# Performance work log

Measured on AMD Instinct MI355X. Metric: run time of the kernel, lower is better.

Reference implementation:

```python
import jax, jax.numpy as jnp
import numpy as np
from jax import lax

GN_EPS = 1e-5
LRELU_SLOPE = 0.2
TOP_K = 3
COMMITMENT = 0.25
NUM_CODES = 1024

def conv(x, w, b, stride=1, pad=1):
    y = lax.conv_general_dilated(x, w, (stride, stride), ((pad, pad), (pad, pad)),
                                 dimension_numbers=('NCHW', 'OIHW', 'NCHW'))
    return y + b[None, :, None, None]

def conv_transpose(x, w, b, stride=2, pad=1, out_pad=1):
    # torch ConvTranspose2d: w is (Cin, Cout, kH, kW); equivalent to lhs-dilated conv
    # with flipped, io-swapped kernel and padding k-1-p (plus out_pad on high side).
    k = w.shape[2]
    p = k - 1 - pad
    w_f = jnp.transpose(jnp.flip(w, (2, 3)), (1, 0, 2, 3))  # -> OIHW
    y = lax.conv_general_dilated(x, w_f, (1, 1), ((p, p + out_pad), (p, p + out_pad)),
                                 lhs_dilation=(stride, stride),
                                 dimension_numbers=('NCHW', 'OIHW', 'NCHW'))
    return y + b[None, :, None, None]

def group_norm(x, g, beta, groups=2):
    N, C, H, W = x.shape
    xg = x.reshape(N, groups, C // groups, H, W)
    mu = xg.mean((2, 3, 4), keepdims=True)
    var = xg.var((2, 3, 4), keepdims=True)
    xn = ((xg - mu) * lax.rsqrt(var + GN_EPS)).reshape(N, C, H, W)
    return xn * g[None, :, None, None] + beta[None, :, None, None]

def lrelu(x):
    return jnp.where(x >= 0, x, LRELU_SLOPE * x)

def vq_ema_eval(z, emb):
    # z: [B, D, H, W] -> tokens [N, D]; eval path (no EMA buffer updates)
    inputs = jnp.transpose(z, (0, 2, 3, 1))  # [B,H,W,D]
    flat = inputs.reshape(-1, emb.shape[1])
    d = (jnp.sum(flat ** 2, 1, keepdims=True) + jnp.sum(emb ** 2, 1)
         - 2.0 * flat @ emb.T)  # [N, K]
    _, idx = lax.top_k(-d, TOP_K)  # top_k smallest distances
    q0 = emb[idx[:, 0]].reshape(inputs.shape)
    e_latent_loss = jnp.mean((lax.stop_gradient(q0) - inputs) ** 2)
    loss = COMMITMENT * e_latent_loss
    quantized = inputs + lax.stop_gradient(q0 - inputs)  # straight-through
    # perplexity uses the LAST (k-th nearest) encodings, matching the torch loop
    last = idx[:, TOP_K - 1]
    counts = jnp.zeros((emb.shape[0],), flat.dtype).at[last].add(1.0)
    avg_probs = counts / flat.shape[0]
    perplexity = jnp.exp(-jnp.sum(avg_probs * jnp.log(avg_probs + 1e-10)))
    return loss, jnp.transpose(quantized, (0, 3, 1, 2)), perplexity

def setup_inputs() -> dict:
    key = jax.random.key(0)
    ks = jax.random.split(key, 16)
    s = 0.05
    d = {
        'x': jax.random.normal(ks[0], (4, 4, 96, 96), jnp.float32),
        'e0_w': jax.random.normal(ks[1], (128, 4, 3, 3), jnp.float32) * s,
        'e0_b': jnp.zeros((128,), jnp.float32),
        'e0_g': jnp.ones((128,), jnp.float32),
        'e0_beta': jnp.zeros((128,), jnp.float32),
        'e1_w': jax.random.normal(ks[2], (128, 128, 3, 3), jnp.float32) * s,
        'e1_b': jnp.zeros((128,), jnp.float32),
        'e1_g': jnp.ones((128,), jnp.float32),
        'e1_beta': jnp.zeros((128,), jnp.float32),
        'pv_w': jax.random.normal(ks[3], (128, 128, 1, 1), jnp.float32) * s,
        'pv_b': jnp.zeros((128,), jnp.float32),
        'emb': jax.random.normal(ks[4], (NUM_CODES, 128), jnp.float32),
        'd0_w': jax.random.normal(ks[5], (128, 128, 3, 3), jnp.float32) * s,  # ConvT: (Cin,Cout,k,k)
        'd0_b': jnp.zeros((128,), jnp.float32),
        'd0_g': jnp.ones((128,), jnp.float32),
        'd0_beta': jnp.zeros((128,), jnp.float32),
        'd1_w': jax.random.normal(ks[6], (128, 256, 3, 3), jnp.float32) * s,
        'd1_b': jnp.zeros((128,), jnp.float32),
        'd1_g': jnp.ones((128,), jnp.float32),
        'd1_beta': jnp.zeros((128,), jnp.float32),
        'proj_w': jax.random.normal(ks[7], (128, 128, 1, 1), jnp.float32) * s,
        'proj_b': jnp.zeros((128,), jnp.float32),
        'ro_w': jax.random.normal(ks[8], (4, 128, 1, 1), jnp.float32) * s,
        'ro_b': jnp.zeros((4,), jnp.float32),
    }
    return d

def reference(x, e0_w, e0_b, e0_g, e0_beta, e1_w, e1_b, e1_g, e1_beta,
              pv_w, pv_b, emb,
              d0_w, d0_b, d0_g, d0_beta, d1_w, d1_b, d1_g, d1_beta,
              proj_w, proj_b, ro_w, ro_b):
    # Encoder: strides [1, 2]
    enc1 = lrelu(group_norm(conv(x, e0_w, e0_b, stride=1, pad=1), e0_g, e0_beta))
    latent = lrelu(group_norm(conv(enc1, e1_w, e1_b, stride=2, pad=1), e1_g, e1_beta))
    z = conv(latent, pv_w, pv_b, stride=1, pad=0)
    loss, quantized, perplexity = vq_ema_eval(z, emb)
    # Decoder: strides [2, 1]; skip projected (embedding_dim != C_out)
    skip = conv(enc1, proj_w, proj_b, stride=1, pad=0)
    h = lrelu(group_norm(conv_transpose(quantized, d0_w, d0_b, stride=2, pad=1, out_pad=1), d0_g, d0_beta))
    y = lrelu(group_norm(conv(jnp.concatenate([h, skip], axis=1), d1_w, d1_b, stride=1, pad=1), d1_g, d1_beta))
    x_recon = conv(y, ro_w, ro_b, stride=1, pad=0)
    return (loss, x_recon, perplexity)
```

## Files before the change

### kernel.cpp

```cpp
#include <hip/hip_runtime.h>

#define DEVI __device__ __forceinline__

typedef unsigned short u16;
typedef __attribute__((ext_vector_type(8))) short bf8v;
typedef __attribute__((ext_vector_type(4))) short s4v;
typedef __attribute__((ext_vector_type(4))) float f4v;

constexpr int NB = 4, C = 128, H = 96, W = 96, HW = H * W;
constexpr int HL = 48, WL = 48, HWL = HL * WL;
constexpr int CODES = 1024, DIM = 128;
constexpr int ROWS = NB * HWL;

DEVI float lrelu_f(float v) { return v >= 0.f ? v : 0.2f * v; }

DEVI u16 f2bf(float f) {
  union { float f; unsigned u; } v; v.f = f;
  unsigned r = (v.u + 0x7FFFu + ((v.u >> 16) & 1u)) >> 16;
  return (u16)r;
}

DEVI float bf2f(u16 h) {
  union { unsigned u; float f; } v; v.u = (unsigned)h << 16;
  return v.f;
}

DEVI void wave_red2(float& s, float& s2) {
#pragma unroll
  for (int o = 32; o > 0; o >>= 1) { s += __shfl_down(s, o); s2 += __shfl_down(s2, o); }
}

DEVI bool block_red2(float& s, float& s2) {
  wave_red2(s, s2);
  __shared__ float ls[8], ls2[8];
  int wv = threadIdx.x >> 6, ln = threadIdx.x & 63;
  if (ln == 0) { ls[wv] = s; ls2[wv] = s2; }
  __syncthreads();
  if (threadIdx.x == 0) {
    s = ls[0] + ls[1] + ls[2] + ls[3];
    s2 = ls2[0] + ls2[1] + ls2[2] + ls2[3];
    return true;
  }
  return false;
}

DEVI void ins3(float e, int j, float& d0, int& i0, float& d1, int& i1, float& d2, int& i2) {
  bool b0 = (e < d0) || (e == d0 && j < i0);
  bool b1 = (e < d1) || (e == d1 && j < i1);
  bool b2 = (e < d2) || (e == d2 && j < i2);
  float nd0 = b0 ? e : d0;             int ni0 = b0 ? j : i0;
  float nd1 = b0 ? d0 : (b1 ? e : d1); int ni1 = b0 ? i0 : (b1 ? j : i1);
  float nd2 = b1 ? d1 : (b2 ? e : d2); int ni2 = b1 ? i1 : (b2 ? j : i2);
  d0 = nd0; i0 = ni0; d1 = nd1; i1 = ni1; d2 = nd2; i2 = ni2;
}

__global__ __launch_bounds__(256) void k_red16(const float2* __restrict__ src,
                                               float* __restrict__ dst, int per) {
  int slot = blockIdx.x;
  float s = 0.f, s2 = 0.f;
  for (int i = threadIdx.x; i < per; i += 256) {
    float2 v = src[(size_t)slot * per + i];
    s += v.x; s2 += v.y;
  }
  if (block_red2(s, s2)) { dst[slot * 2] = s; dst[slot * 2 + 1] = s2; }
}

__global__ __launch_bounds__(256) void k_pack_all(
    const float* __restrict__ d1_w, const float* __restrict__ d0_w,
    const float* __restrict__ pj_w, const float* __restrict__ emb,
    u16* __restrict__ A1, u16* __restrict__ A0, u16* __restrict__ Apj,
    u16* __restrict__ ehlp, float* __restrict__ enorm, float* __restrict__ counts) {
  int b = blockIdx.x, t = threadIdx.x;
  if (b < 1152) {
    int i = b * 256 + t;
    int ci = i & 31, co = (i >> 5) & 127, r = i >> 12;
    int kx = r % 3; int r2 = r / 3; int ch = r2 & 7, ky = r2 >> 3;
    A1[i] = f2bf(d1_w[((size_t)(co * 256 + ch * 32 + ci) * 3 + ky) * 3 + kx]);
  } else if (b < 1728) {
    int i = (b - 1152) * 256 + t;
    int ci = i & 31, co = (i >> 5) & 127, r = i >> 12;
    int wx = r % 3; int r2 = r / 3; int ch = r2 & 3, wy = r2 >> 2;
    A0[i] = f2bf(d0_w[((size_t)((ch * 32 + ci) * 128 + co) * 3 + wy) * 3 + wx]);
  } else if (b < 1792) {
    int i = (b - 1728) * 256 + t;
    int ci = i & 31, co = (i >> 5) & 127, ch = i >> 12;
    Apj[i] = f2bf(pj_w[co * 128 + ch * 32 + ci]);
  } else if (b < 1920) {
    int i = (b - 1792) * 256 + t;
    int k4 = i & 31, code = i >> 5;
    float4 e = *(const float4*)&emb[(size_t)code * DIM + k4 * 4];
    u16 h0 = f2bf(e.x), h1 = f2bf(e.y), h2 = f2bf(e.z), h3 = f2bf(e.w);
    u16 l0 = f2bf(e.x - bf2f(h0)), l1 = f2bf(e.y - bf2f(h1));
    u16 l2 = f2bf(e.z - bf2f(h2)), l3 = f2bf(e.w - bf2f(h3));
    s4v hv = {(short)h0, (short)h1, (short)h2, (short)h3};
    s4v lv = {(short)l0, (short)l1, (short)l2, (short)l3};
    *(s4v*)&ehlp[(size_t)code * 256 + k4 * 4] = hv;
    *(s4v*)&ehlp[(size_t)code * 256 + 128 + k4 * 4] = lv;
  } else if (b < 1924) {
    int e = (b - 1920) * 256 + t;
    const float4* p = (const float4*)(emb + (size_t)e * DIM);
    float s = 0.f;
#pragma unroll 8
    for (int i = 0; i < 32; ++i) {
      float4 v = p[i];
      s = fmaf(v.x, v.x, s); s = fmaf(v.y, v.y, s); s = fmaf(v.z, v.z, s); s = fmaf(v.w, v.w, s);
    }
    enorm[e] = s;
  } else {
#pragma unroll
    for (int k = 0; k < 4; ++k) counts[t + k * 256] = 0.f;
  }
}

__global__ __launch_bounds__(256) void k_conv_e0t(
    const float* __restrict__ x, const float* __restrict__ wg,
    const float* __restrict__ bias, float* __restrict__ out, float2* __restrict__ ps) {
  __shared__ float xs[4][18][104];
  int b = blockIdx.x;
  int rq = b % 6; int co = (b / 6) & 127; int n = b / 768;
  int t = threadIdx.x;
  int tx = t & 15, r = t >> 4;
  int y0 = rq * 16;
  for (int e = t; e < 4 * 18 * 104; e += 256) {
    int ci = e / 1872; int rem = e - ci * 1872;
    int row = rem / 104; int off = rem - row * 104;
    int iy = y0 - 1 + row; int ix = off - 1;
    float v = 0.f;
    if ((unsigned)iy < 96u && (unsigned)ix < 96u)
      v = x[((size_t)(n * 4 + ci)) * HW + iy * 96 + ix];
    xs[ci][row][off] = v;
  }
  float wr[4][9];
  const float* wp = wg + co * 36;
#pragma unroll
  for (int ci = 0; ci < 4; ++ci)
#pragma unroll
    for (int k = 0; k < 9; ++k) wr[ci][k] = wp[ci * 9 + k];
  float bv = bias[co];
  __syncthreads();
  float acc[6];
#pragma unroll
  for (int p = 0; p < 6; ++p) acc[p] = bv;
#pragma unroll
  for (int ci = 0; ci < 4; ++ci) {
#pragma unroll
    for (int ky = 0; ky < 3; ++ky) {
      const float* rp = &xs[ci][r + ky][6 * tx];
      float f[8];
#pragma unroll
      for (int j = 0; j < 4; ++j) {
        float2 v2 = *(const float2*)(rp + 2 * j);
        f[2 * j] = v2.x; f[2 * j + 1] = v2.y;
      }
      float w0 = wr[ci][ky * 3 + 0], w1 = wr[ci][ky * 3 + 1], w2 = wr[ci][ky * 3 + 2];
#pragma unroll
      for (int p = 0; p < 6; ++p)
        acc[p] = fmaf(w0, f[p], fmaf(w1, f[p + 1], fmaf(w2, f[p + 2], acc[p])));
    }
  }
  float* op = out + ((size_t)(n * 128 + co) * 96 + (y0 + r)) * 96 + 6 * tx;
#pragma unroll
  for (int j = 0; j < 3; ++j) {
    float2 v2 = { acc[2 * j], acc[2 * j + 1] };
    *(float2*)(op + 2 * j) = v2;
  }
  float s = 0.f, s2 = 0.f;
#pragma unroll
  for (int p = 0; p < 6; ++p) { s += acc[p]; s2 += acc[p] * acc[p]; }
  if (block_red2(s, s2)) {
    int slot = n * 2 + (co >> 6);
    ps[(size_t)slot * 384 + (co & 63) * 6 + rq] = make_float2(s, s2);
  }
}

__global__ __launch_bounds__(256) void k_gn_pad(
    const float* __restrict__ in, const float* __restrict__ stats,
    const float* __restrict__ gam, const float* __restrict__ bet, float* __restrict__ outp) {
  int idx = blockIdx.x * 256 + threadIdx.x;
  int col = idx % 100; int r2 = idx / 100; int row = r2 % 98; int c2 = r2 / 98;
  int c = c2 & 127; int n = c2 >> 7;
  float v = 0.f;
  if (row >= 1 && row <= 96 && col >= 1 && col <= 96) {
    const float* st = stats + (n * 2 + (c >> 6)) * 2;
    const float invc = 1.f / (64.f * 9216.f);
    float mu = st[0] * invc;
    float var = fmaf(-mu, mu, st[1] * invc);
    float rs = rsqrtf(var + 1e-5f);
    float raw = in[(size_t)c2 * 9216 + (row - 1) * 96 + (col - 1)];
    v = lrelu_f(fmaf((raw - mu) * rs, gam[c], bet[c]));
  }
  outp[idx] = v;
}

__global__ __launch_bounds__(256) void k_gn_nhwc_bf(
    const float* __restrict__ in, u16* __restrict__ outb, const float* __restrict__ stats,
    const float* __restrict__ gam, const float* __restrict__ bet) {
  int idx = blockIdx.x * 256 + threadIdx.x;
  int c = idx & 127;
  int n = idx / (9216 * 128);
  const float* st = stats + (n * 2 + (c >> 6)) * 2;
  const float invcnt = 1.f / (64.f * 9216.f);
  float mu = st[0] * invcnt;
  float var = fmaf(-mu, mu, st[1] * invcnt);
  float rs = rsqrtf(var + 1e-5f);
  float v = in[idx];
  outb[idx] = f2bf(lrelu_f(fmaf((v - mu) * rs, gam[c], bet[c])));
}

__global__ __launch_bounds__(256, 4) void k_conv_e1s(
    const float* __restrict__ gnpad, const float* __restrict__ wg, float* __restrict__ part) {
  __shared__ float insh[8 * 500];
  __shared__ float wsh[8 * 576];
  int b = blockIdx.x;
  int cb = b & 1; int kb = (b >> 1) & 3; int rq = (b >> 3) % 24; int n = b / 192;
  int co0 = cb * 64;
  int t = threadIdx.x;
  int tx = t & 15, r = (t >> 4) & 1, cg = t >> 5;
  float acc[8][3];
#pragma unroll
  for (int c = 0; c < 8; ++c)
#pragma unroll
    for (int p = 0; p < 3; ++p) acc[c][p] = 0.f;
  for (int cc = 0; cc < 4; ++cc) {
    __syncthreads();
    const float4* src = (const float4*)(gnpad + ((size_t)(n * 128 + kb * 32 + cc * 8)) * 9800 + 4 * rq * 100);
#pragma unroll
    for (int j = 0; j < 4; ++j) {
      int e = t + j * 256;
      if (e < 1000) {
        int ci = e / 125; int q = e - ci * 125;
        *(float4*)&insh[ci * 500 + q * 4] = src[(size_t)ci * 2450 + q];
      }
    }
#pragma unroll
    for (int j = 0; j < 18; ++j) {
      int e = t + j * 256;
      int ci = e / 576; int rem = e - ci * 576; int k = rem >> 6; int co = rem & 63;
      wsh[e] = wg[(size_t)(co0 + co) * 1152 + (kb * 32 + cc * 8 + ci) * 9 + k];
    }
    __syncthreads();
#pragma unroll
    for (int ci = 0; ci < 8; ++ci) {
      float iv[3][3][3];
      int ib = ci * 500 + (2 * r) * 100 + 2 * tx;
#pragma unroll
      for (int ky = 0; ky < 3; ++ky) {
#pragma unroll
        for (int p = 0; p < 3; ++p) {
          int a = ib + ky * 100 + 32 * p;
          float2 v2 = *(const float2*)&insh[a];
          iv[ky][p][0] = v2.x; iv[ky][p][1] = v2.y; iv[ky][p][2] = insh[a + 2];
        }
      }
#pragma unroll
      for (int k = 0; k < 9; ++k) {
        float4 wa = *(const float4*)&wsh[ci * 576 + k * 64 + cg * 8];
        float4 wb = *(const float4*)&wsh[ci * 576 + k * 64 + cg * 8 + 4];
        int ky = k / 3, kx = k - ky * 3;
#pragma unroll
        for (int p = 0; p < 3; ++p) {
          float ivv = iv[ky][p][kx];
          acc[0][p] = fmaf(wa.x, ivv, acc[0][p]);
          acc[1][p] = fmaf(wa.y, ivv, acc[1][p]);
          acc[2][p] = fmaf(wa.z, ivv, acc[2][p]);
          acc[3][p] = fmaf(wa.w, ivv, acc[3][p]);
          acc[4][p] = fmaf(wb.x, ivv, acc[4][p]);
          acc[5][p] = fmaf(wb.y, ivv, acc[5][p]);
          acc[6][p] = fmaf(wb.z, ivv, acc[6][p]);
          acc[7][p] = fmaf(wb.w, ivv, acc[7][p]);
        }
      }
    }
  }
  int oy = 2 * rq + r;
#pragma unroll
  for (int c = 0; c < 8; ++c) {
    size_t ob = (size_t)kb * 1179648 + ((size_t)(n * 128 + co0 + cg * 8 + c)) * HWL + oy * 48 + tx;
#pragma unroll
    for (int p = 0; p < 3; ++p) part[ob + 16 * p] = acc[c][p];
  }
}

__global__ __launch_bounds__(256) void k_e1comb(
    const float* __restrict__ part, const float* __restrict__ bias,
    float* __restrict__ latent, float2* __restrict__ ps) {
  int idx = blockIdx.x * 256 + threadIdx.x;
  int c = (idx / HWL) & 127;
  int n = idx / (HWL * 128);
  float v = part[idx] + part[idx + 1179648] + part[idx + 2 * 1179648] + part[idx + 3 * 1179648] + bias[c];
  latent[idx] = v;
  float s = v, s2 = v * v;
  if (block_red2(s, s2)) {
    int slot = n * 2 + (c >> 6);
    int j = blockIdx.x % 9;
    ps[(size_t)slot * 576 + (c & 63) * 9 + j] = make_float2(s, s2);
  }
}

__global__ __launch_bounds__(256, 2) void k_pv(
    const float* __restrict__ in, const float* __restrict__ w,
    const float* __restrict__ bias, const float* __restrict__ stats1,
    const float* __restrict__ gam, const float* __restrict__ bet,
    u16* __restrict__ zp) {
  int b = blockIdx.x;
  int pxb = b % 36; int cb = (b / 36) & 1; int n = b / 72;
  int t = threadIdx.x;
  int pxg = t & 7, cg = t >> 3;
  int px0 = pxb * 64 + pxg * 8;
  int cobase = cb * 64 + cg * 2;
  const float invc = 1.f / (64.f * 2304.f);
  float acc[2][8];
#pragma unroll
  for (int c = 0; c < 2; ++c) {
    float bv = bias[cobase + c];
#pragma unroll
    for (int p = 0; p < 8; ++p) acc[c][p] = bv;
  }
  const float* ipb = in + (size_t)n * 128 * HWL + px0;
  for (int ci0 = 0; ci0 < 128; ci0 += 4) {
    float inr[4][8];
#pragma unroll
    for (int i = 0; i < 4; ++i) {
      int c = ci0 + i;
      const float* st = stats1 + (n * 2 + (c >> 6)) * 2;
      float mu = st[0] * invc;
      float var = fmaf(-mu, mu, st[1] * invc);
      float rsv = rsqrtf(var + 1e-5f);
      float ga = gam[c], be = bet[c];
      const float* ip = ipb + (size_t)c * HWL;
      float4 a = *(const float4*)ip; float4 bq = *(const float4*)(ip + 4);
      inr[i][0] = lrelu_f(fmaf((a.x - mu) * rsv, ga, be));
      inr[i][1] = lrelu_f(fmaf((a.y - mu) * rsv, ga, be));
      inr[i][2] = lrelu_f(fmaf((a.z - mu) * rsv, ga, be));
      inr[i][3] = lrelu_f(fmaf((a.w - mu) * rsv, ga, be));
      inr[i][4] = lrelu_f(fmaf((bq.x - mu) * rsv, ga, be));
      inr[i][5] = lrelu_f(fmaf((bq.y - mu) * rsv, ga, be));
      inr[i][6] = lrelu_f(fmaf((bq.z - mu) * rsv, ga, be));
      inr[i][7] = lrelu_f(fmaf((bq.w - mu) * rsv, ga, be));
    }
    float wr[2][4];
#pragma unroll
    for (int c = 0; c < 2; ++c) {
      float4 wv = *(const float4*)&w[(size_t)(cobase + c) * 128 + ci0];
      wr[c][0] = wv.x; wr[c][1] = wv.y; wr[c][2] = wv.z; wr[c][3] = wv.w;
    }
#pragma unroll
    for (int i = 0; i < 4; ++i)
#pragma unroll
      for (int c = 0; c < 2; ++c)
#pragma unroll
        for (int p = 0; p < 8; ++p) acc[c][p] = fmaf(wr[c][i], inr[i][p], acc[c][p]);
  }
#pragma unroll
  for (int p = 0; p < 8; ++p) {
    size_t r = (size_t)n * HWL + px0 + p;
    u16 h0 = f2bf(acc[0][p]); u16 l0 = f2bf(acc[0][p] - bf2f(h0));
    u16 h1 = f2bf(acc[1][p]); u16 l1 = f2bf(acc[1][p] - bf2f(h1));
    unsigned hp = (unsigned)h0 | ((unsigned)h1 << 16);
    unsigned lp = (unsigned)l0 | ((unsigned)l1 << 16);
    *(unsigned*)&zp[r * 256 + cobase] = hp;
    *(unsigned*)&zp[r * 256 + 128 + cobase] = lp;
  }
}

__global__ __launch_bounds__(256) void k_vq(
    const u16* __restrict__ zp, const u16* __restrict__ ehlp,
    const float* __restrict__ emb, const float* __restrict__ enorm,
    u16* __restrict__ qb, float* __restrict__ counts, float* __restrict__ pvq) {
  __shared__ float wd[4][16][3];
  __shared__ int   wi[4][16][3];
  __shared__ float lred[4];
  __shared__ int hist[CODES];
  int r0 = blockIdx.x * 16;
  int t = threadIdx.x, w = t >> 6, lane = t & 63;
  int ln16 = lane & 15, quad = lane >> 4;
#pragma unroll
  for (int k = 0; k < 4; ++k) hist[t + k * 256] = 0;
  const u16* zrow = zp + (size_t)(r0 + ln16) * 256 + quad * 8;
  bf8v bh[4], bl[4];
#pragma unroll
  for (int kk = 0; kk < 4; ++kk) {
    bh[kk] = *(const bf8v*)(zrow + kk * 32);
    bl[kk] = *(const bf8v*)(zrow + 128 + kk * 32);
  }
  float d0 = 3.4e38f, d1 = 3.4e38f, d2 = 3.4e38f;
  int i0 = -1, i1 = -1, i2 = -1;
  const u16* abase = ehlp + (size_t)(w * 256 + ln16) * 256 + quad * 8;
  for (int ct = 0; ct < 16; ++ct) {
    const u16* ap = abase + (size_t)ct * 16 * 256;
    bf8v af[8];
#pragma unroll
    for (int kk = 0; kk < 8; ++kk) af[kk] = *(const bf8v*)(ap + kk * 32);
    f4v accA = (f4v){0.f, 0.f, 0.f, 0.f};
    f4v accB = (f4v){0.f, 0.f, 0.f, 0.f};
    f4v accC = (f4v){0.f, 0.f, 0.f, 0.f};
#pragma unroll
    for (int kk = 0; kk < 4; ++kk) {
      accA = __builtin_amdgcn_mfma_f32_16x16x32_bf16(af[kk], bh[kk], accA, 0, 0, 0);
      accB = __builtin_amdgcn_mfma_f32_16x16x32_bf16(af[4 + kk], bh[kk], accB, 0, 0, 0);
      accC = __builtin_amdgcn_mfma_f32_16x16x32_bf16(af[kk], bl[kk], accC, 0, 0, 0);
    }
    int cbase = w * 256 + ct * 16 + quad * 4;
#pragma unroll
    for (int g = 0; g < 4; ++g) {
      int code = cbase + g;
      float dot = accA[g] + accB[g] + accC[g];
      float d = fmaf(-2.f, dot, enorm[code]);
      bool b0 = d < d0, b1 = d < d1, b2 = d < d2;
      float nd0 = b0 ? d : d0;             int ni0 = b0 ? code : i0;
      float nd1 = b0 ? d0 : (b1 ? d : d1); int ni1 = b0 ? i0 : (b1 ? code : i1);
      float nd2 = b1 ? d1 : (b2 ? d : d2); int ni2 = b1 ? i1 : (b2 ? code : i2);
      d0 = nd0; i0 = ni0; d1 = nd1; i1 = ni1; d2 = nd2; i2 = ni2;
    }
  }
#pragma unroll
  for (int off = 16; off <= 32; off <<= 1) {
    float e0 = __shfl_xor(d0, off), e1 = __shfl_xor(d1, off), e2 = __shfl_xor(d2, off);
    int j0 = __shfl_xor(i0, off), j1 = __shfl_xor(i1, off), j2 = __shfl_xor(i2, off);
    ins3(e0, j0, d0, i0, d1, i1, d2, i2);
    ins3(e1, j1, d0, i0, d1, i1, d2, i2);
    ins3(e2, j2, d0, i0, d1, i1, d2, i2);
  }
  if (quad == 0) {
    wd[w][ln16][0] = d0; wd[w][ln16][1] = d1; wd[w][ln16][2] = d2;
    wi[w][ln16][0] = i0; wi[w][ln16][1] = i1; wi[w][ln16][2] = i2;
  }
  __syncthreads();
  float lsum = 0.f;
  for (int ii = 0; ii < 4; ++ii) {
    int i = w * 4 + ii;
    float m0 = wd[0][i][0], m1 = wd[0][i][1], m2 = wd[0][i][2];
    int a0 = wi[0][i][0], a1 = wi[0][i][1], a2 = wi[0][i][2];
#pragma unroll
    for (int q = 1; q < 4; ++q) {
      ins3(wd[q][i][0], wi[q][i][0], m0, a0, m1, a1, m2, a2);
      ins3(wd[q][i][1], wi[q][i][1], m0, a0, m1, a1, m2, a2);
      ins3(wd[q][i][2], wi[q][i][2], m0, a0, m1, a1, m2, a2);
    }
    int r = r0 + i;
    const float* q0p = emb + (size_t)a0 * DIM;
    const u16* zr = zp + (size_t)r * 256;
    float lp = 0.f;
#pragma unroll
    for (int cc = 0; cc < 2; ++cc) {
      int c = lane + cc * 64;
      float qv = q0p[c];
      qb[(size_t)r * 128 + c] = f2bf(qv);
      float zv = bf2f(zr[c]) + bf2f(zr[128 + c]);
      float dd = zv - qv;
      lp = fmaf(dd, dd, lp);
    }
#pragma unroll
    for (int o = 32; o > 0; o >>= 1) lp += __shfl_down(lp, o);
    if (lane == 0) { lsum += lp; atomicAdd(&hist[a2], 1); }
  }
  if (lane == 0) lred[w] = lsum;
  __syncthreads();
  if (t == 0) pvq[blockIdx.x] = lred[0] + lred[1] + lred[2] + lred[3];
#pragma unroll
  for (int k = 0; k < 4; ++k) {
    int e = t + k * 256;
    int cnt = hist[e];
    if (cnt) atomicAdd(&counts[e], (float)cnt);
  }
}

__global__ __launch_bounds__(256) void k_finalize(
    const float* __restrict__ counts, const float* __restrict__ pvq, float* __restrict__ out) {
  float local = 0.f;
#pragma unroll
  for (int k = 0; k < 4; ++k) {
    float cnt = counts[threadIdx.x + k * 256];
    float pr = cnt * (1.f / (float)ROWS);
    local = fmaf(pr, logf(pr + 1e-10f), local);
  }
  float lsum = 0.f;
  for (int i = threadIdx.x; i < ROWS / 16; i += 256) lsum += pvq[i];
  if (block_red2(local, lsum)) {
    out[1 + NB * 4 * HW] = expf(-local);
    out[0] = 0.25f * lsum * (1.f / (9216.f * 128.f));
  }
}

__global__ __launch_bounds__(256) void k_proj_m(
    const float* __restrict__ enc1, const u16* __restrict__ Apj,
    const float* __restrict__ bias, const float* __restrict__ stats0,
    const float* __restrict__ gam, const float* __restrict__ bet,
    u16* __restrict__ skipb) {
  __shared__ u16 Ash[128 * 32];
  __shared__ u16 Bsh[96 * 32];
  int b = blockIdx.x; int rowi = b % 96; int n = b / 96; int px0 = rowi * 96;
  int t = threadIdx.x; int w = t >> 6; int lane = t & 63;
  int ln16 = lane & 15, quad = lane >> 4;
  int co0w = (w & 1) * 64; int pxh = (w >> 1) * 48;
  int c_l = t & 31, xg = t >> 5;
  const float invc = 1.f / (64.f * 9216.f);
  f4v acc[4][3];
#pragma unroll
  for (int mt = 0; mt < 4; ++mt)
#pragma unroll
    for (int nt = 0; nt < 3; ++nt) acc[mt][nt] = (f4v){0.f, 0.f, 0.f, 0.f};
  for (int ch = 0; ch < 4; ++ch) {
    __syncthreads();
#pragma unroll
    for (int e = 0; e < 2; ++e) {
      int i = t + e * 256;
      *(bf8v*)&Ash[i * 8] = *(const bf8v*)&Apj[ch * 4096 + i * 8];
    }
    int c = ch * 32 + c_l;
    const float* st = stats0 + (n * 2 + (ch >> 1)) * 2;
    float mu = st[0] * invc;
    float var = fmaf(-mu, mu, st[1] * invc);
    float rsv = rsqrtf(var + 1e-5f);
    float ga = gam[c], be = bet[c];
    const float* ip = enc1 + (size_t)(n * 128 + c) * 9216 + px0 + xg * 12;
#pragma unroll
    for (int j4 = 0; j4 < 3; ++j4) {
      float4 v = *(const float4*)(ip + j4 * 4);
      int pxb = xg * 12 + j4 * 4;
      Bsh[(pxb + 0) * 32 + c_l] = f2bf(lrelu_f(fmaf((v.x - mu) * rsv, ga, be)));
      Bsh[(pxb + 1) * 32 + c_l] = f2bf(lrelu_f(fmaf((v.y - mu) * rsv, ga, be)));
      Bsh[(pxb + 2) * 32 + c_l] = f2bf(lrelu_f(fmaf((v.z - mu) * rsv, ga, be)));
      Bsh[(pxb + 3) * 32 + c_l] = f2bf(lrelu_f(fmaf((v.w - mu) * rsv, ga, be)));
    }
    __syncthreads();
    bf8v af[4];
#pragma unroll
    for (int mt = 0; mt < 4; ++mt)
      af[mt] = *(const bf8v*)&Ash[(co0w + mt * 16 + ln16) * 32 + quad * 8];
#pragma unroll
    for (int nt = 0; nt < 3; ++nt) {
      bf8v bfv = *(const bf8v*)&Bsh[(pxh + nt * 16 + ln16) * 32 + quad * 8];
#pragma unroll
      for (int mt = 0; mt < 4; ++mt)
        acc[mt][nt] = __builtin_amdgcn_mfma_f32_16x16x32_bf16(af[mt], bfv, acc[mt][nt], 0, 0, 0);
    }
  }
#pragma unroll
  for (int mt = 0; mt < 4; ++mt) {
    int co = co0w + mt * 16 + quad * 4;
    float4 bv = *(const float4*)&bias[co];
#pragma unroll
    for (int nt = 0; nt < 3; ++nt) {
      int px = px0 + pxh + nt * 16 + ln16;
      u16* dp = skipb + (size_t)(n * 9216 + px) * 128 + co;
      s4v sv;
      sv.x = (short)f2bf(acc[mt][nt].x + bv.x);
      sv.y = (short)f2bf(acc[mt][nt].y + bv.y);
      sv.z = (short)f2bf(acc[mt][nt].z + bv.z);
      sv.w = (short)f2bf(acc[mt][nt].w + bv.w);
      *(s4v*)dp = sv;
    }
  }
}

__global__ __launch_bounds__(256) void k_convt_d0m(
    const u16* __restrict__ qb, const u16* __restrict__ A0,
    const float* __restrict__ bias, float* __restrict__ h, float2* __restrict__ ps) {
  __shared__ u16 Ash[2 * 128 * 32];
  __shared__ u16 Bsh[49 * 32];
  int b = blockIdx.x; int rx = b & 1; int oy = (b >> 1) % 96; int n = b / 192;
  int t = threadIdx.x; int w = t >> 6; int lane = t & 63;
  int ln16 = lane & 15, quad = lane >> 4;
  int co0w = w * 32;
  f4v acc[2][3];
#pragma unroll
  for (int mt = 0; mt < 2; ++mt)
#pragma unroll
    for (int nt = 0; nt < 3; ++nt) acc[mt][nt] = (f4v){0.f, 0.f, 0.f, 0.f};
  int nyt, wys[2], iys[2];
  if (oy & 1) {
    wys[0] = 2; iys[0] = (oy - 1) >> 1;
    wys[1] = 0; iys[1] = (oy + 1) >> 1;
    nyt = (iys[1] < 48) ? 2 : 1;
  } else { wys[0] = 1; iys[0] = oy >> 1; wys[1] = 0; iys[1] = 0; nyt = 1; }
  int nxt = rx ? 2 : 1;
  int wxs[2], xof[2];
  if (rx) { wxs[0] = 2; xof[0] = 0; wxs[1] = 0; xof[1] = 1; }
  else { wxs[0] = 1; xof[0] = 0; wxs[1] = 0; xof[1] = 0; }
  for (int yt = 0; yt < nyt; ++yt) {
    for (int ch = 0; ch < 4; ++ch) {
      __syncthreads();
      for (int e = t; e < nxt * 512; e += 256) {
        int xt = e >> 9, e2 = e & 511;
        const u16* Asrc = A0 + (size_t)(((wys[yt] * 4 + ch) * 3 + wxs[xt]) * 4096);
        *(bf8v*)&Ash[xt * 4096 + e2 * 8] = *(const bf8v*)&Asrc[e2 * 8];
      }
      const u16* bbase = qb + (size_t)(n * 2304 + iys[yt] * 48) * 128 + ch * 32;
      for (int e = t; e < 196; e += 256) {
        int row = e >> 2, seg = e & 3;
        bf8v v = {0, 0, 0, 0, 0, 0, 0, 0};
        if (row < 48) v = *(const bf8v*)&bbase[row * 128 + seg * 8];
        *(bf8v*)&Bsh[row * 32 + seg * 8] = v;
      }
      __syncthreads();
      for (int xt = 0; xt < nxt; ++xt) {
        bf8v af[2];
#pragma unroll
        for (int mt = 0; mt < 2; ++mt)
          af[mt] = *(const bf8v*)&Ash[xt * 4096 + (co0w + mt * 16 + ln16) * 32 + quad * 8];
#pragma unroll
        for (int nt = 0; nt < 3; ++nt) {
          bf8v bfv = *(const bf8v*)&Bsh[(nt * 16 + ln16 + xof[xt]) * 32 + quad * 8];
#pragma unroll
          for (int mt = 0; mt < 2; ++mt)
            acc[mt][nt] = __builtin_amdgcn_mfma_f32_16x16x32_bf16(af[mt], bfv, acc[mt][nt], 0, 0, 0);
        }
      }
    }
  }
  float s = 0.f, s2 = 0.f;
#pragma unroll
  for (int mt = 0; mt < 2; ++mt) {
    int co = co0w + mt * 16 + quad * 4;
    float4 bv = *(const float4*)&bias[co];
#pragma unroll
    for (int nt = 0; nt < 3; ++nt) {
      int px = nt * 16 + ln16;
      int ox = 2 * px + rx;
      float4 v;
      v.x = acc[mt][nt].x + bv.x; v.y = acc[mt][nt].y + bv.y;
      v.z = acc[mt][nt].z + bv.z; v.w = acc[mt][nt].w + bv.w;
      *(float4*)(h + (size_t)(n * 9216 + oy * 96 + ox) * 128 + co) = v;
      s += v.x + v.y + v.z + v.w;
      s2 += v.x * v.x + v.y * v.y + v.z * v.z + v.w * v.w;
    }
  }
  wave_red2(s, s2);
  if (lane == 0) {
    int slot = n * 2 + (w >> 1);
    ps[(size_t)slot * 384 + (oy * 2 + rx) * 2 + (w & 1)] = make_float2(s, s2);
  }
}

__global__ __launch_bounds__(256) void k_conv_d1m(
    const u16* __restrict__ hb, const u16* __restrict__ sb,
    const u16* __restrict__ A1, const float* __restrict__ bias,
    float* __restrict__ y, float2* __restrict__ ps) {
  __shared__ u16 Ash[3 * 64 * 32];
  __shared__ u16 Bsh[98 * 32];
  int b = blockIdx.x; int cb = b & 1; int oy = (b >> 1) % 96; int n = b / 192;
  int t = threadIdx.x; int w = t >> 6; int lane = t & 63;
  int ln16 = lane & 15, quad = lane >> 4;
  int co0w = (w & 1) * 32; int pxh = (w >> 1) * 48;
  f4v acc[2][3];
#pragma unroll
  for (int mt = 0; mt < 2; ++mt)
#pragma unroll
    for (int nt = 0; nt < 3; ++nt) acc[mt][nt] = (f4v){0.f, 0.f, 0.f, 0.f};
  int ky0 = (oy == 0) ? 1 : 0, ky1 = (oy == 95) ? 1 : 2;
  for (int ky = ky0; ky <= ky1; ++ky) {
    int iy = oy + ky - 1;
    for (int ch = 0; ch < 8; ++ch) {
      const u16* src = (ch < 4) ? hb : sb;
      int c0 = (ch & 3) * 32;
      const u16* Asrc = A1 + (size_t)(ky * 8 + ch) * 12288;
      const u16* bbase = src + (size_t)(n * 9216 + iy * 96) * 128 + c0;
      __syncthreads();
#pragma unroll
      for (int j = 0; j < 3; ++j) {
        int e = t + j * 256;
        int kx = e >> 8; int e2 = e & 255; int co_l = e2 >> 2; int seg = e2 & 3;
        *(bf8v*)&Ash[(kx * 64 + co_l) * 32 + seg * 8] =
            *(const bf8v*)&Asrc[(size_t)kx * 4096 + (cb * 64 + co_l) * 32 + seg * 8];
      }
      for (int e = t; e < 392; e += 256) {
        int row = e >> 2, seg = e & 3;
        int ix = row - 1;
        bf8v v = {0, 0, 0, 0, 0, 0, 0, 0};
        if ((unsigned)ix < 96u) v = *(const bf8v*)&bbase[ix * 128 + seg * 8];
        *(bf8v*)&Bsh[row * 32 + seg * 8] = v;
      }
      __syncthreads();
#pragma unroll
      for (int kx = 0; kx < 3; ++kx) {
        bf8v af[2];
#pragma unroll
        for (int mt = 0; mt < 2; ++mt)
          af[mt] = *(const bf8v*)&Ash[(kx * 64 + co0w + mt * 16 + ln16) * 32 + quad * 8];
#pragma unroll
        for (int nt = 0; nt < 3; ++nt) {
          bf8v bfv = *(const bf8v*)&Bsh[(pxh + nt * 16 + ln16 + kx) * 32 + quad * 8];
#pragma unroll
          for (int mt = 0; mt < 2; ++mt)
            acc[mt][nt] = __builtin_amdgcn_mfma_f32_16x16x32_bf16(af[mt], bfv, acc[mt][nt], 0, 0, 0);
        }
      }
    }
  }
  float s = 0.f, s2 = 0.f;
#pragma unroll
  for (int mt = 0; mt < 2; ++mt) {
    int co = cb * 64 + co0w + mt * 16 + quad * 4;
    float4 bv = *(const float4*)&bias[co];
#pragma unroll
    for (int nt = 0; nt < 3; ++nt) {
      int px = pxh + nt * 16 + ln16;
      float4 v;
      v.x = acc[mt][nt].x + bv.x; v.y = acc[mt][nt].y + bv.y;
      v.z = acc[mt][nt].z + bv.z; v.w = acc[mt][nt].w + bv.w;
      *(float4*)(y + (size_t)(n * 9216 + oy * 96 + px) * 128 + co) = v;
      s += v.x + v.y + v.z + v.w;
      s2 += v.x * v.x + v.y * v.y + v.z * v.z + v.w * v.w;
    }
  }
  wave_red2(s, s2);
  if (lane == 0) {
    int slot = n * 2 + cb;
    ps[(size_t)slot * 384 + oy * 4 + w] = make_float2(s, s2);
  }
}

__global__ __launch_bounds__(256) void k_ro(
    const float* __restrict__ y, const float* __restrict__ w,
    const float* __restrict__ bias, const float* __restrict__ stats3,
    const float* __restrict__ gam, const float* __restrict__ bet,
    float* __restrict__ out) {
  __shared__ float wsh[512];
  __shared__ float gsh[128], bsh[128];
  __shared__ float red[64][16];
  int b = blockIdx.x; int n = b / 144; int px0 = (b % 144) * 64;
  int t = threadIdx.x; int q = t & 3, pxl = t >> 2;
  for (int e = t; e < 512; e += 256) wsh[e] = w[e];
  if (t < 128) { gsh[t] = gam[t]; bsh[t] = bet[t]; }
  __syncthreads();
  const float invc = 1.f / (64.f * 9216.f);
  int g = q >> 1;
  const float* st = stats3 + (n * 2 + g) * 2;
  float mu = st[0] * invc;
  float var = fmaf(-mu, mu, st[1] * invc);
  float rsv = rsqrtf(var + 1e-5f);
  const float* yb = y + (size_t)(n * 9216 + px0 + pxl) * 128 + q * 32;
  float s0 = 0.f, s1 = 0.f, s2 = 0.f, s3 = 0.f;
#pragma unroll
  for (int j = 0; j < 8; ++j) {
    float4 v = *(const float4*)(yb + j * 4);
    int c0 = q * 32 + j * 4;
    float vx = lrelu_f(fmaf((v.x - mu) * rsv, gsh[c0 + 0], bsh[c0 + 0]));
    float vy = lrelu_f(fmaf((v.y - mu) * rsv, gsh[c0 + 1], bsh[c0 + 1]));
    float vz = lrelu_f(fmaf((v.z - mu) * rsv, gsh[c0 + 2], bsh[c0 + 2]));
    float vw = lrelu_f(fmaf((v.w - mu) * rsv, gsh[c0 + 3], bsh[c0 + 3]));
    const float* w0 = &wsh[0 * 128 + c0];
    const float* w1 = &wsh[1 * 128 + c0];
    const float* w2 = &wsh[2 * 128 + c0];
    const float* w3 = &wsh[3 * 128 + c0];
    s0 += vx * w0[0] + vy * w0[1] + vz * w0[2] + vw * w0[3];
    s1 += vx * w1[0] + vy * w1[1] + vz * w1[2] + vw * w1[3];
    s2 += vx * w2[0] + vy * w2[1] + vz * w2[2] + vw * w2[3];
    s3 += vx * w3[0] + vy * w3[1] + vz * w3[2] + vw * w3[3];
  }
  red[pxl][q * 4 + 0] = s0; red[pxl][q * 4 + 1] = s1;
  red[pxl][q * 4 + 2] = s2; red[pxl][q * 4 + 3] = s3;
  __syncthreads();
  float val = red[pxl][0 * 4 + q] + red[pxl][1 * 4 + q] + red[pxl][2 * 4 + q] + red[pxl][3 * 4 + q] + bias[q];
  out[1 + (size_t)(n * 4 + q) * 9216 + px0 + pxl] = val;
}

extern "C" void kernel_launch(void* const* d_in, const int* in_sizes, int n_in,
                              void* d_out, int out_size, void* d_ws, size_t ws_size,
                              hipStream_t stream) {
  (void)in_sizes; (void)n_in; (void)out_size; (void)ws_size;
  const float* x     = (const float*)d_in[0];
  const float* e0_w  = (const float*)d_in[1];
  const float* e0_b  = (const float*)d_in[2];
  const float* e0_g  = (const float*)d_in[3];
  const float* e0_bt = (const float*)d_in[4];
  const float* e1_w  = (const float*)d_in[5];
  const float* e1_b  = (const float*)d_in[6];
  const float* e1_g  = (const float*)d_in[7];
  const float* e1_bt = (const float*)d_in[8];
  const float* pv_w  = (const float*)d_in[9];
  const float* pv_b  = (const float*)d_in[10];
  const float* emb   = (const float*)d_in[11];
  const float* d0_w  = (const float*)d_in[12];
  const float* d0_b  = (const float*)d_in[13];
  const float* d0_g  = (const float*)d_in[14];
  const float* d0_bt = (const float*)d_in[15];
  const float* d1_w  = (const float*)d_in[16];
  const float* d1_b  = (const float*)d_in[17];
  const float* d1_g  = (const float*)d_in[18];
  const float* d1_bt = (const float*)d_in[19];
  const float* pj_w  = (const float*)d_in[20];
  const float* pj_b  = (const float*)d_in[21];
  const float* ro_w  = (const float*)d_in[22];
  const float* ro_b  = (const float*)d_in[23];
  float* out = (float*)d_out;
  float* ws = (float*)d_ws;

  float* stats  = ws;
  float* counts = ws + 64;
  float* enorm  = ws + 1088;
  float* pvq    = ws + 2112;
  float2* ps_e0 = (float2*)(ws + 3264);
  float2* ps_e1 = (float2*)(ws + 76992);
  float2* ps_d0 = (float2*)(ws + 95424);
  float2* ps_d1 = (float2*)(ws + 107712);
  float* enc1   = ws + 114688;
  float* latent = enc1 + (size_t)NB * C * HW;
  float* zbuf   = latent + (size_t)NB * C * HWL;
  float* hy     = zbuf + (size_t)NB * C * HWL;
  u16* qb    = (u16*)(hy + (size_t)NB * C * HW);
  u16* hb    = qb + (size_t)NB * C * HWL;
  u16* skipb = hb + (size_t)NB * C * HW;
  u16* A1    = skipb + (size_t)NB * C * HW;
  u16* A0    = A1 + 294912;
  u16* Apj   = A0 + 147456;
  u16* ehlp  = Apj + 16384 + 64;
  u16* zp    = (u16*)zbuf;
  float* gnpad = (float*)qb;

  k_pack_all<<<1925, 256, 0, stream>>>(d1_w, d0_w, pj_w, emb, A1, A0, Apj, ehlp, enorm, counts);

  k_conv_e0t<<<3072, 256, 0, stream>>>(x, e0_w, e0_b, enc1, ps_e0);
  k_red16<<<8, 256, 0, stream>>>(ps_e0, stats + 0, 384);
  k_gn_pad<<<512 * 9800 / 256, 256, 0, stream>>>(enc1, stats + 0, e0_g, e0_bt, gnpad);
  k_conv_e1s<<<768, 256, 0, stream>>>(gnpad, e1_w, hy);
  k_e1comb<<<NB * C * HWL / 256, 256, 0, stream>>>(hy, e1_b, latent, ps_e1);
  k_red16<<<8, 256, 0, stream>>>(ps_e1, stats + 16, 576);
  k_pv<<<288, 256, 0, stream>>>(latent, pv_w, pv_b, stats + 16, e1_g, e1_bt, zp);
  k_vq<<<ROWS / 16, 256, 0, stream>>>(zp, ehlp, emb, enorm, qb, counts, pvq);
  k_finalize<<<1, 256, 0, stream>>>(counts, pvq, out);

  k_proj_m<<<NB * 96, 256, 0, stream>>>(enc1, Apj, pj_b, stats + 0, e0_g, e0_bt, skipb);
  k_convt_d0m<<<NB * 96 * 2, 256, 0, stream>>>(qb, A0, d0_b, hy, ps_d0);
  k_red16<<<8, 256, 0, stream>>>(ps_d0, stats + 32, 384);
  k_gn_nhwc_bf<<<NB * C * HW / 256, 256, 0, stream>>>(hy, hb, stats + 32, d0_g, d0_bt);
  k_conv_d1m<<<NB * 96 * 2, 256, 0, stream>>>(hb, skipb, A1, d1_b, hy, ps_d1);
  k_red16<<<8, 256, 0, stream>>>(ps_d1, stats + 48, 384);
  k_ro<<<NB * 144, 256, 0, stream>>>(hy, ro_w, ro_b, stats + 48, d1_g, d1_bt, out);
}
```

Measured before the change: 396.8 us.

## Tile codebook in MFMA fragment order and widen VQ blocks to 16 waves

The codebook hi/lo bf16 copy is now packed in MFMA fragment order, so each lane's 8-element load is contiguous and coalesced across the wave. The VQ kernel moves from 4 to 16 waves per block, and each wave scans 64 codes instead of 256. The cross-wave top-3 merge becomes a wave-level shuffle argmin repeated three times, one row per wave. This raises parallelism and load efficiency per block, at the cost of 1024-thread blocks with a single-block launch bound, plus changed tie-breaking in the merge.

```diff
diff --git a/kernel.cpp b/kernel.cpp
--- a/kernel.cpp
+++ b/kernel.cpp
@@ -69,7 +69,7 @@
     const float* __restrict__ d1_w, const float* __restrict__ d0_w,
     const float* __restrict__ pj_w, const float* __restrict__ emb,
     u16* __restrict__ A1, u16* __restrict__ A0, u16* __restrict__ Apj,
-    u16* __restrict__ ehlp, float* __restrict__ enorm, float* __restrict__ counts) {
+    u16* __restrict__ ehtil, float* __restrict__ enorm, float* __restrict__ counts) {
   int b = blockIdx.x, t = threadIdx.x;
   if (b < 1152) {
     int i = b * 256 + t;
@@ -86,16 +86,23 @@
     int ci = i & 31, co = (i >> 5) & 127, ch = i >> 12;
     Apj[i] = f2bf(pj_w[co * 128 + ch * 32 + ci]);
   } else if (b < 1920) {
-    int i = (b - 1792) * 256 + t;
-    int k4 = i & 31, code = i >> 5;
-    float4 e = *(const float4*)&emb[(size_t)code * DIM + k4 * 4];
-    u16 h0 = f2bf(e.x), h1 = f2bf(e.y), h2 = f2bf(e.z), h3 = f2bf(e.w);
-    u16 l0 = f2bf(e.x - bf2f(h0)), l1 = f2bf(e.y - bf2f(h1));
-    u16 l2 = f2bf(e.z - bf2f(h2)), l3 = f2bf(e.w - bf2f(h3));
-    s4v hv = {(short)h0, (short)h1, (short)h2, (short)h3};
-    s4v lv = {(short)l0, (short)l1, (short)l2, (short)l3};
-    *(s4v*)&ehlp[(size_t)code * 256 + k4 * 4] = hv;
-    *(s4v*)&ehlp[(size_t)code * 256 + 128 + k4 * 4] = lv;
+    int g = (b - 1792) * 256 + t;
+    int ct = g >> 9; int rem = g & 511;
+    int j = rem >> 6; int l = rem & 63;
+    int code = ct * 16 + (l & 15);
+    int kb = j * 32 + (l >> 4) * 8;
+    bool lo = kb >= 128; int k0 = lo ? kb - 128 : kb;
+    const float* ep = emb + (size_t)code * DIM + k0;
+    u16 o[8];
+#pragma unroll
+    for (int e = 0; e < 8; ++e) {
+      float v = ep[e];
+      u16 h = f2bf(v);
+      o[e] = lo ? f2bf(v - bf2f(h)) : h;
+    }
+    bf8v ov = {(short)o[0], (short)o[1], (short)o[2], (short)o[3],
+               (short)o[4], (short)o[5], (short)o[6], (short)o[7]};
+    *(bf8v*)&ehtil[(size_t)g * 8] = ov;
   } else if (b < 1924) {
     int e = (b - 1920) * 256 + t;
     const float4* p = (const float4*)(emb + (size_t)e * DIM);
@@ -363,19 +370,18 @@
   }
 }
 
-__global__ __launch_bounds__(256) void k_vq(
-    const u16* __restrict__ zp, const u16* __restrict__ ehlp,
+__global__ __launch_bounds__(1024, 1) void k_vq(
+    const u16* __restrict__ zp, const u16* __restrict__ ehtil,
     const float* __restrict__ emb, const float* __restrict__ enorm,
     u16* __restrict__ qb, float* __restrict__ counts, float* __restrict__ pvq) {
-  __shared__ float wd[4][16][3];
-  __shared__ int   wi[4][16][3];
-  __shared__ float lred[4];
+  __shared__ float wd[16][16][3];
+  __shared__ int   wi[16][16][3];
+  __shared__ float lred[16];
   __shared__ int hist[CODES];
   int r0 = blockIdx.x * 16;
   int t = threadIdx.x, w = t >> 6, lane = t & 63;
   int ln16 = lane & 15, quad = lane >> 4;
-#pragma unroll
-  for (int k = 0; k < 4; ++k) hist[t + k * 256] = 0;
+  hist[t] = 0;
   const u16* zrow = zp + (size_t)(r0 + ln16) * 256 + quad * 8;
   bf8v bh[4], bl[4];
 #pragma unroll
@@ -385,12 +391,13 @@
   }
   float d0 = 3.4e38f, d1 = 3.4e38f, d2 = 3.4e38f;
   int i0 = -1, i1 = -1, i2 = -1;
-  const u16* abase = ehlp + (size_t)(w * 256 + ln16) * 256 + quad * 8;
-  for (int ct = 0; ct < 16; ++ct) {
-    const u16* ap = abase + (size_t)ct * 16 * 256;
+  const u16* abase = ehtil + (size_t)(w * 4) * 4096 + lane * 8;
+#pragma unroll
+  for (int tt = 0; tt < 4; ++tt) {
+    const u16* ap = abase + tt * 4096;
     bf8v af[8];
 #pragma unroll
-    for (int kk = 0; kk < 8; ++kk) af[kk] = *(const bf8v*)(ap + kk * 32);
+    for (int j = 0; j < 8; ++j) af[j] = *(const bf8v*)(ap + j * 512);
     f4v accA = (f4v){0.f, 0.f, 0.f, 0.f};
     f4v accB = (f4v){0.f, 0.f, 0.f, 0.f};
     f4v accC = (f4v){0.f, 0.f, 0.f, 0.f};
@@ -400,7 +407,7 @@
       accB = __builtin_amdgcn_mfma_f32_16x16x32_bf16(af[4 + kk], bh[kk], accB, 0, 0, 0);
       accC = __builtin_amdgcn_mfma_f32_16x16x32_bf16(af[kk], bl[kk], accC, 0, 0, 0);
     }
-    int cbase = w * 256 + ct * 16 + quad * 4;
+    int cbase = (w * 4 + tt) * 16 + quad * 4;
 #pragma unroll
     for (int g = 0; g < 4; ++g) {
       int code = cbase + g;
@@ -426,43 +433,46 @@
     wi[w][ln16][0] = i0; wi[w][ln16][1] = i1; wi[w][ln16][2] = i2;
   }
   __syncthreads();
-  float lsum = 0.f;
-  for (int ii = 0; ii < 4; ++ii) {
-    int i = w * 4 + ii;
-    float m0 = wd[0][i][0], m1 = wd[0][i][1], m2 = wd[0][i][2];
-    int a0 = wi[0][i][0], a1 = wi[0][i][1], a2 = wi[0][i][2];
-#pragma unroll
-    for (int q = 1; q < 4; ++q) {
-      ins3(wd[q][i][0], wi[q][i][0], m0, a0, m1, a1, m2, a2);
-      ins3(wd[q][i][1], wi[q][i][1], m0, a0, m1, a1, m2, a2);
-      ins3(wd[q][i][2], wi[q][i][2], m0, a0, m1, a1, m2, a2);
-    }
-    int r = r0 + i;
-    const float* q0p = emb + (size_t)a0 * DIM;
-    const u16* zr = zp + (size_t)r * 256;
-    float lp = 0.f;
-#pragma unroll
-    for (int cc = 0; cc < 2; ++cc) {
-      int c = lane + cc * 64;
-      float qv = q0p[c];
-      qb[(size_t)r * 128 + c] = f2bf(qv);
-      float zv = bf2f(zr[c]) + bf2f(zr[128 + c]);
-      float dd = zv - qv;
-      lp = fmaf(dd, dd, lp);
-    }
-#pragma unroll
-    for (int o = 32; o > 0; o >>= 1) lp += __shfl_down(lp, o);
-    if (lane == 0) { lsum += lp; atomicAdd(&hist[a2], 1); }
-  }
-  if (lane == 0) lred[w] = lsum;
+  float bd; int bi;
+  if (lane < 48) { bd = wd[lane / 3][w][lane % 3]; bi = wi[lane / 3][w][lane % 3]; }
+  else { bd = 3.4e38f; bi = 0x7fffffff; }
+  int a[3];
+#pragma unroll
+  for (int p = 0; p < 3; ++p) {
+    float d = bd; int i = bi;
+#pragma unroll
+    for (int o = 1; o <= 32; o <<= 1) {
+      float od = __shfl_xor(d, o); int oi = __shfl_xor(i, o);
+      if (od < d || (od == d && oi < i)) { d = od; i = oi; }
+    }
+    a[p] = i;
+    if (bi == i) { bd = 3.4e38f; bi = 0x7fffffff; }
+  }
+  int r = r0 + w;
+  const float* q0p = emb + (size_t)a[0] * DIM;
+  const u16* zr = zp + (size_t)r * 256;
+  float lp = 0.f;
+#pragma unroll
+  for (int cc = 0; cc < 2; ++cc) {
+    int c = lane + cc * 64;
+    float qv = q0p[c];
+    qb[(size_t)r * 128 + c] = f2bf(qv);
+    float zv = bf2f(zr[c]) + bf2f(zr[128 + c]);
+    float dd = zv - qv;
+    lp = fmaf(dd, dd, lp);
+  }
+#pragma unroll
+  for (int o = 32; o > 0; o >>= 1) lp += __shfl_down(lp, o);
+  if (lane == 0) { lred[w] = lp; atomicAdd(&hist[a[2]], 1); }
   __syncthreads();
-  if (t == 0) pvq[blockIdx.x] = lred[0] + lred[1] + lred[2] + lred[3];
-#pragma unroll
-  for (int k = 0; k < 4; ++k) {
-    int e = t + k * 256;
-    int cnt = hist[e];
-    if (cnt) atomicAdd(&counts[e], (float)cnt);
-  }
+  if (t == 0) {
+    float s = 0.f;
+#pragma unroll
+    for (int q = 0; q < 16; ++q) s += lred[q];
+    pvq[blockIdx.x] = s;
+  }
+  int cnt = hist[t];
+  if (cnt) atomicAdd(&counts[t], (float)cnt);
 }
 
 __global__ __launch_bounds__(256) void k_finalize(
@@ -805,11 +815,11 @@
   u16* A1    = skipb + (size_t)NB * C * HW;
   u16* A0    = A1 + 294912;
   u16* Apj   = A0 + 147456;
-  u16* ehlp  = Apj + 16384 + 64;
+  u16* ehtil = Apj + 16384 + 64;
   u16* zp    = (u16*)zbuf;
   float* gnpad = (float*)qb;
 
-  k_pack_all<<<1925, 256, 0, stream>>>(d1_w, d0_w, pj_w, emb, A1, A0, Apj, ehlp, enorm, counts);
+  k_pack_all<<<1925, 256, 0, stream>>>(d1_w, d0_w, pj_w, emb, A1, A0, Apj, ehtil, enorm, counts);
 
   k_conv_e0t<<<3072, 256, 0, stream>>>(x, e0_w, e0_b, enc1, ps_e0);
   k_red16<<<8, 256, 0, stream>>>(ps_e0, stats + 0, 384);
@@ -818,7 +828,7 @@
   k_e1comb<<<NB * C * HWL / 256, 256, 0, stream>>>(hy, e1_b, latent, ps_e1);
   k_red16<<<8, 256, 0, stream>>>(ps_e1, stats + 16, 576);
   k_pv<<<288, 256, 0, stream>>>(latent, pv_w, pv_b, stats + 16, e1_g, e1_bt, zp);
-  k_vq<<<ROWS / 16, 256, 0, stream>>>(zp, ehlp, emb, enorm, qb, counts, pvq);
+  k_vq<<<ROWS / 16, 1024, 0, stream>>>(zp, ehtil, emb, enorm, qb, counts, pvq);
   k_finalize<<<1, 256, 0, stream>>>(counts, pvq, out);
 
   k_proj_m<<<NB * 96, 256, 0, stream>>>(enc1, Apj, pj_b, stats + 0, e0_g, e0_bt, skipb);
```

New measurement: 384.0 us. 1.03x faster.
